# Optimization experiments

Hardware: AMD Instinct MI355X
Metric: run time of the kernel (lower is better)

Reference implementation:

```python
import jax, jax.numpy as jnp
import numpy as np

B, N, C, H, W = 32, 8, 256, 4, 4


def setup_inputs() -> dict:
    key = jax.random.key(0)
    k1, k2 = jax.random.split(key)
    pred = jax.random.normal(k1, (B, N, C, H, W), dtype=jnp.float32)
    gt = jax.random.normal(k2, (B, N, C, H, W), dtype=jnp.float32)
    return {"pred": pred, "gt": gt}


def reference(pred, gt):
    b, n, c, h, w = pred.shape
    M = b * n * h * w
    # (B,N,C,H,W) -> (B,N,H,W,C) -> (M, C)
    p = jnp.transpose(pred, (0, 1, 3, 4, 2)).reshape(M, c)
    # (B,N,C,H,W) -> (C,B,N,H,W) -> (C, M)
    g = jnp.transpose(gt, (2, 0, 1, 3, 4)).reshape(c, M)
    lossmat = p @ g  # (M, M) similarity matrix
    # CrossEntropy with target = arange(M): -mean(log_softmax diag)
    logp = jax.nn.log_softmax(lossmat, axis=1)
    loss = -jnp.mean(jnp.diagonal(logp))
    # accuracy (no grad in original)
    top1 = jnp.argmax(lossmat, axis=1)
    acc = jnp.mean((top1 == jnp.arange(M)).astype(jnp.float32)) * 100.0
    return (loss, acc)
```

## Files before the change

### kernel.cpp

```cpp
#include <hip/hip_runtime.h>
#include <cstdint>

typedef __bf16 bf16x8 __attribute__((ext_vector_type(8)));
typedef float floatx4 __attribute__((ext_vector_type(4)));


#define OFF_X     (0u)
#define OFF_Y     (2u*1024*1024)
#define OFF_PMAX  (4u*1024*1024)
#define OFF_PSUM  (5u*1024*1024)
#define OFF_DIAG  (6u*1024*1024)
#define OFF_LPART (OFF_DIAG + 16384u)
#define OFF_CPART (OFF_LPART + 256u)

#define AS1C(p) ((const __attribute__((address_space(1))) void*)(const void*)(p))
#define AS3(p)  ((__attribute__((address_space(3))) void*)(void*)(p))

__global__ __launch_bounds__(256) void transpose_stage(
    const float* __restrict__ pred, const float* __restrict__ gt,
    unsigned short* __restrict__ Xs, unsigned short* __restrict__ Ys) {
  int blk = blockIdx.x;
  const float* src;
  unsigned short* dst;
  int slab;
  if (blk < 256) { src = pred; dst = Xs; slab = blk; }
  else           { src = gt;   dst = Ys; slab = blk - 256; }
  const float* sb = src + slab * 4096;
  const int rb = slab >> 3, rowhi = slab & 7;
  const int t = threadIdx.x;
  #pragma unroll
  for (int half = 0; half < 2; ++half) {
    int c_ = half * 256 + t;
    int rowlo = c_ & 15;
    int quad  = (c_ >> 4) & 3;
    int kk    = (c_ >> 6) & 1;
    int s     = c_ >> 7;
    int k0 = s * 64 + kk * 32 + quad * 8;
    unsigned int packed[4];
    #pragma unroll
    for (int jj = 0; jj < 4; ++jj) {
      unsigned int lohi[2];
      #pragma unroll
      for (int e = 0; e < 2; ++e) {
        float f = sb[(k0 + jj * 2 + e) * 16 + rowlo];
        unsigned int u = __float_as_uint(f);
        lohi[e] = (u + 0x7FFFu + ((u >> 16) & 1u)) >> 16;
      }
      packed[jj] = lohi[0] | (lohi[1] << 16);
    }
    unsigned short* o = dst + rb * 32768 +
        (unsigned)(s * 1024 + kk * 512 + rowhi * 64 + quad * 16 + rowlo) * 8;
    uint4 v; v.x = packed[0]; v.y = packed[1]; v.z = packed[2]; v.w = packed[3];
    *reinterpret_cast<uint4*>(o) = v;
  }
}

__global__ __launch_bounds__(256) void gemm_softmax_partial(
    const unsigned short* __restrict__ Xs, const unsigned short* __restrict__ Ys,
    float* __restrict__ pmax, float* __restrict__ psum, float* __restrict__ diag) {
  __shared__ __align__(16) unsigned short As[8192];
  __shared__ __align__(16) unsigned short Bs[8192];
  const int t = threadIdx.x;
  const int wave = t >> 6, lane = t & 63;
  const int rg = wave >> 1, cg = wave & 1;
  const int bR = blockIdx.x, bC = blockIdx.y;
  const unsigned short* Ag = Xs + bR * 32768;
  const unsigned short* Bg = Ys + bC * 32768;

  floatx4 acc[4][4];
  const floatx4 zero = {0.f, 0.f, 0.f, 0.f};
  #pragma unroll
  for (int i = 0; i < 4; ++i)
    #pragma unroll
    for (int j = 0; j < 4; ++j) acc[i][j] = zero;

  for (int s = 0; s < 4; ++s) {
    #pragma unroll
    for (int it = 0; it < 4; ++it) {
      int chunk = it * 256 + t;
      __builtin_amdgcn_global_load_lds(AS1C(Ag + s * 8192 + chunk * 8),
                                       AS3(As + chunk * 8), 16, 0, 0);
      __builtin_amdgcn_global_load_lds(AS1C(Bg + s * 8192 + chunk * 8),
                                       AS3(Bs + chunk * 8), 16, 0, 0);
    }
    __syncthreads();
    #pragma unroll
    for (int kk = 0; kk < 2; ++kk) {
      bf16x8 a[4], b[4];
      #pragma unroll
      for (int fr = 0; fr < 4; ++fr)
        a[fr] = *reinterpret_cast<const bf16x8*>(
            As + (unsigned)(kk * 512 + (rg * 4 + fr) * 64 + lane) * 8);
      #pragma unroll
      for (int fc = 0; fc < 4; ++fc)
        b[fc] = *reinterpret_cast<const bf16x8*>(
            Bs + (unsigned)(kk * 512 + (cg * 4 + fc) * 64 + lane) * 8);
      #pragma unroll
      for (int fr = 0; fr < 4; ++fr)
        #pragma unroll
        for (int fc = 0; fc < 4; ++fc)
          acc[fr][fc] = __builtin_amdgcn_mfma_f32_16x16x32_bf16(
              a[fr], b[fc], acc[fr][fc], 0, 0, 0);
    }
    if (s < 3) __syncthreads();
  }

  const int quad = lane >> 4, lc = lane & 15;

  if (bR == bC && rg == cg) {
    #pragma unroll
    for (int fr = 0; fr < 4; ++fr)
      #pragma unroll
      for (int r = 0; r < 4; ++r)
        if (lc == quad * 4 + r)
          diag[bR * 128 + rg * 64 + fr * 16 + lc] = acc[fr][fr][r];
  }

  #pragma unroll
  for (int fr = 0; fr < 4; ++fr) {
    #pragma unroll
    for (int r = 0; r < 4; ++r) {
      float v0 = acc[fr][0][r], v1 = acc[fr][1][r];
      float v2 = acc[fr][2][r], v3 = acc[fr][3][r];
      float m = fmaxf(fmaxf(v0, v1), fmaxf(v2, v3));
      #pragma unroll
      for (int sh = 1; sh < 16; sh <<= 1) m = fmaxf(m, __shfl_xor(m, sh, 64));
      float ss = __expf(v0 - m) + __expf(v1 - m) +
                 __expf(v2 - m) + __expf(v3 - m);
      #pragma unroll
      for (int sh = 1; sh < 16; sh <<= 1) ss += __shfl_xor(ss, sh, 64);
      if (lc == 0) {
        int grow = bR * 128 + rg * 64 + fr * 16 + quad * 4 + r;
        int p = grow * 64 + bC * 2 + cg;
        pmax[p] = m; psum[p] = ss;
      }
    }
  }
}

__global__ __launch_bounds__(256) void combine_rows(
    const float* __restrict__ pmax, const float* __restrict__ psum,
    const float* __restrict__ diag,
    float* __restrict__ lpart, float* __restrict__ cpart) {
  int row = blockIdx.x * 256 + threadIdx.x;
  const float* pm = pmax + row * 64;
  const float* ps = psum + row * 64;
  float M = -3.4e38f;
  #pragma unroll 8
  for (int b = 0; b < 64; ++b) M = fmaxf(M, pm[b]);
  float S = 0.f;
  #pragma unroll 8
  for (int b = 0; b < 64; ++b) S += ps[b] * __expf(pm[b] - M);
  float d = diag[row];
  float lossr = logf(S) + M - d;
  float corr = (d == M) ? 1.f : 0.f;
  #pragma unroll
  for (int sh = 1; sh < 64; sh <<= 1) {
    lossr += __shfl_xor(lossr, sh, 64);
    corr  += __shfl_xor(corr,  sh, 64);
  }
  __shared__ float ls[4], cs[4];
  int wave = threadIdx.x >> 6, lane = threadIdx.x & 63;
  if (lane == 0) { ls[wave] = lossr; cs[wave] = corr; }
  __syncthreads();
  if (threadIdx.x == 0) {
    lpart[blockIdx.x] = ls[0] + ls[1] + ls[2] + ls[3];
    cpart[blockIdx.x] = cs[0] + cs[1] + cs[2] + cs[3];
  }
}

__global__ void finalize(const float* __restrict__ lpart,
                         const float* __restrict__ cpart,
                         float* __restrict__ out) {
  int t = threadIdx.x;
  float l = (t < 16) ? lpart[t] : 0.f;
  float c = (t < 16) ? cpart[t] : 0.f;
  #pragma unroll
  for (int sh = 1; sh < 16; sh <<= 1) {
    l += __shfl_xor(l, sh, 64);
    c += __shfl_xor(c, sh, 64);
  }
  if (t == 0) {
    out[0] = l * (1.f / 4096.f);
    out[1] = c * (100.f / 4096.f);
  }
}

extern "C" void kernel_launch(void* const* d_in, const int* in_sizes, int n_in,
                              void* d_out, int out_size, void* d_ws, size_t ws_size,
                              hipStream_t stream) {
  const float* pred = (const float*)d_in[0];
  const float* gt   = (const float*)d_in[1];
  char* w = (char*)d_ws;
  unsigned short* Xbf = (unsigned short*)(w + OFF_X);
  unsigned short* Ybf = (unsigned short*)(w + OFF_Y);
  float* pmax  = (float*)(w + OFF_PMAX);
  float* psum  = (float*)(w + OFF_PSUM);
  float* diag  = (float*)(w + OFF_DIAG);
  float* lpart = (float*)(w + OFF_LPART);
  float* cpart = (float*)(w + OFF_CPART);
  float* out   = (float*)d_out;

  transpose_stage<<<512, 256, 0, stream>>>(pred, gt, Xbf, Ybf);
  dim3 g1(32, 32);
  gemm_softmax_partial<<<g1, 256, 0, stream>>>(Xbf, Ybf, pmax, psum, diag);
  combine_rows<<<16, 256, 0, stream>>>(pmax, psum, diag, lpart, cpart);
  finalize<<<1, 64, 0, stream>>>(lpart, cpart, out);
}
```

Measured before the change: 94.22 us.

## Fuse row combine and finalize into GEMM kernel via last-block atomic counters

Removes the separate combine_rows and finalize launches. Each GEMM block bumps a per-row-block atomic counter, and the last block to finish a row block does the log-sum-exp combine for its 128 rows. A second counter then lets the final block sum the partials and write the outputs. The transpose kernel zeroes the counters, and the GEMM gains a launch_bounds occupancy hint. This saves two kernel launches in exchange for fences, atomics and a serial tail on the last blocks.

Result: slower. 123.6 us (+31.2%).

```diff
diff --git a/kernel.cpp b/kernel.cpp
--- a/kernel.cpp
+++ b/kernel.cpp
@@ -12,14 +12,18 @@
 #define OFF_DIAG  (6u*1024*1024)
 #define OFF_LPART (OFF_DIAG + 16384u)
 #define OFF_CPART (OFF_LPART + 256u)
+#define OFF_CNT   (OFF_CPART + 256u)
 
 #define AS1C(p) ((const __attribute__((address_space(1))) void*)(const void*)(p))
 #define AS3(p)  ((__attribute__((address_space(3))) void*)(void*)(p))
 
 __global__ __launch_bounds__(256) void transpose_stage(
     const float* __restrict__ pred, const float* __restrict__ gt,
-    unsigned short* __restrict__ Xs, unsigned short* __restrict__ Ys) {
+    unsigned short* __restrict__ Xs, unsigned short* __restrict__ Ys,
+    int* __restrict__ cnt) {
   int blk = blockIdx.x;
+  const int t = threadIdx.x;
+  if (blk == 0 && t < 33) cnt[t] = 0;
   const float* src;
   unsigned short* dst;
   int slab;
@@ -27,7 +31,6 @@
   else           { src = gt;   dst = Ys; slab = blk - 256; }
   const float* sb = src + slab * 4096;
   const int rb = slab >> 3, rowhi = slab & 7;
-  const int t = threadIdx.x;
   #pragma unroll
   for (int half = 0; half < 2; ++half) {
     int c_ = half * 256 + t;
@@ -55,11 +58,15 @@
   }
 }
 
-__global__ __launch_bounds__(256) void gemm_softmax_partial(
+__global__ __launch_bounds__(256, 4) void gemm_softmax_combine(
     const unsigned short* __restrict__ Xs, const unsigned short* __restrict__ Ys,
-    float* __restrict__ pmax, float* __restrict__ psum, float* __restrict__ diag) {
+    float* __restrict__ pmax, float* __restrict__ psum, float* __restrict__ diag,
+    float* __restrict__ lpart, float* __restrict__ cpart,
+    int* __restrict__ cnt, float* __restrict__ out) {
   __shared__ __align__(16) unsigned short As[8192];
   __shared__ __align__(16) unsigned short Bs[8192];
+  __shared__ float ls[4], cs[4];
+  __shared__ int lastflag;
   const int t = threadIdx.x;
   const int wave = t >> 6, lane = t & 63;
   const int rg = wave >> 1, cg = wave & 1;
@@ -136,53 +143,52 @@
       }
     }
   }
-}
-
-__global__ __launch_bounds__(256) void combine_rows(
-    const float* __restrict__ pmax, const float* __restrict__ psum,
-    const float* __restrict__ diag,
-    float* __restrict__ lpart, float* __restrict__ cpart) {
-  int row = blockIdx.x * 256 + threadIdx.x;
-  const float* pm = pmax + row * 64;
-  const float* ps = psum + row * 64;
-  float M = -3.4e38f;
-  #pragma unroll 8
-  for (int b = 0; b < 64; ++b) M = fmaxf(M, pm[b]);
-  float S = 0.f;
-  #pragma unroll 8
-  for (int b = 0; b < 64; ++b) S += ps[b] * __expf(pm[b] - M);
-  float d = diag[row];
-  float lossr = logf(S) + M - d;
-  float corr = (d == M) ? 1.f : 0.f;
+
+  __syncthreads();
+  if (t == 0) {
+    __threadfence();
+    int old = atomicAdd(cnt + bR, 1);
+    lastflag = (old == 31) ? 1 : 0;
+  }
+  __syncthreads();
+  if (!lastflag) return;
+
+  __threadfence();
+
+  float lossr = 0.f, corr = 0.f;
+  if (t < 128) {
+    int row = bR * 128 + t;
+    const float* pm = pmax + row * 64;
+    const float* ps = psum + row * 64;
+    float M = -3.4e38f;
+    #pragma unroll 8
+    for (int b = 0; b < 64; ++b) M = fmaxf(M, pm[b]);
+    float S = 0.f;
+    #pragma unroll 8
+    for (int b = 0; b < 64; ++b) S += ps[b] * __expf(pm[b] - M);
+    float d = diag[row];
+    lossr = logf(S) + M - d;
+    corr = (d == M) ? 1.f : 0.f;
+  }
   #pragma unroll
   for (int sh = 1; sh < 64; sh <<= 1) {
     lossr += __shfl_xor(lossr, sh, 64);
     corr  += __shfl_xor(corr,  sh, 64);
   }
-  __shared__ float ls[4], cs[4];
-  int wave = threadIdx.x >> 6, lane = threadIdx.x & 63;
   if (lane == 0) { ls[wave] = lossr; cs[wave] = corr; }
   __syncthreads();
-  if (threadIdx.x == 0) {
-    lpart[blockIdx.x] = ls[0] + ls[1] + ls[2] + ls[3];
-    cpart[blockIdx.x] = cs[0] + cs[1] + cs[2] + cs[3];
-  }
-}
-
-__global__ void finalize(const float* __restrict__ lpart,
-                         const float* __restrict__ cpart,
-                         float* __restrict__ out) {
-  int t = threadIdx.x;
-  float l = (t < 16) ? lpart[t] : 0.f;
-  float c = (t < 16) ? cpart[t] : 0.f;
-  #pragma unroll
-  for (int sh = 1; sh < 16; sh <<= 1) {
-    l += __shfl_xor(l, sh, 64);
-    c += __shfl_xor(c, sh, 64);
-  }
   if (t == 0) {
-    out[0] = l * (1.f / 4096.f);
-    out[1] = c * (100.f / 4096.f);
+    lpart[bR] = ls[0] + ls[1] + ls[2] + ls[3];
+    cpart[bR] = cs[0] + cs[1] + cs[2] + cs[3];
+    __threadfence();
+    int old2 = atomicAdd(cnt + 32, 1);
+    if (old2 == 31) {
+      __threadfence();
+      float L = 0.f, C = 0.f;
+      for (int i = 0; i < 32; ++i) { L += lpart[i]; C += cpart[i]; }
+      out[0] = L * (1.f / 4096.f);
+      out[1] = C * (100.f / 4096.f);
+    }
   }
 }
 
@@ -199,11 +205,11 @@
   float* diag  = (float*)(w + OFF_DIAG);
   float* lpart = (float*)(w + OFF_LPART);
   float* cpart = (float*)(w + OFF_CPART);
+  int*   cnt   = (int*)(w + OFF_CNT);
   float* out   = (float*)d_out;
 
-  transpose_stage<<<512, 256, 0, stream>>>(pred, gt, Xbf, Ybf);
+  transpose_stage<<<512, 256, 0, stream>>>(pred, gt, Xbf, Ybf, cnt);
   dim3 g1(32, 32);
-  gemm_softmax_partial<<<g1, 256, 0, stream>>>(Xbf, Ybf, pmax, psum, diag);
-  combine_rows<<<16, 256, 0, stream>>>(pmax, psum, diag, lpart, cpart);
-  finalize<<<1, 64, 0, stream>>>(lpart, cpart, out);
+  gemm_softmax_combine<<<g1, 256, 0, stream>>>(Xbf, Ybf, pmax, psum, diag,
+                                               lpart, cpart, cnt, out);
 }
```

## Enlarge GEMM tiles to 256x256 with double-buffered LDS and fuse finalize

Applied to the files above, without the earlier changes.

The GEMM moves from 128x128 tiles with 4 waves to 256x256 tiles with 8 waves per block, so each block reuses more operand data, and it double-buffers the LDS loads so the next K-slab is fetched while the current one runs on MFMA. The separate finalize kernel is removed: the last combine_rows block, detected through an atomic counter reset in the transpose kernel, sums the partials and writes the output. The grid drops to 256 blocks, which may underfill the CUs, and LDS use rises to 128KB per block.

New measurement: 94.06 us. About the same (-0.2%).

```diff
diff --git a/kernel.cpp b/kernel.cpp
--- a/kernel.cpp
+++ b/kernel.cpp
@@ -12,14 +12,18 @@
 #define OFF_DIAG  (6u*1024*1024)
 #define OFF_LPART (OFF_DIAG + 16384u)
 #define OFF_CPART (OFF_LPART + 256u)
+#define OFF_CNT   (OFF_CPART + 256u)
 
 #define AS1C(p) ((const __attribute__((address_space(1))) void*)(const void*)(p))
 #define AS3(p)  ((__attribute__((address_space(3))) void*)(void*)(p))
 
 __global__ __launch_bounds__(256) void transpose_stage(
     const float* __restrict__ pred, const float* __restrict__ gt,
-    unsigned short* __restrict__ Xs, unsigned short* __restrict__ Ys) {
+    unsigned short* __restrict__ Xs, unsigned short* __restrict__ Ys,
+    int* __restrict__ cnt) {
   int blk = blockIdx.x;
+  const int t = threadIdx.x;
+  if (blk == 0 && t < 33) cnt[t] = 0;
   const float* src;
   unsigned short* dst;
   int slab;
@@ -27,7 +31,6 @@
   else           { src = gt;   dst = Ys; slab = blk - 256; }
   const float* sb = src + slab * 4096;
   const int rb = slab >> 3, rowhi = slab & 7;
-  const int t = threadIdx.x;
   #pragma unroll
   for (int half = 0; half < 2; ++half) {
     int c_ = half * 256 + t;
@@ -55,69 +58,83 @@
   }
 }
 
-__global__ __launch_bounds__(256) void gemm_softmax_partial(
+__global__ __launch_bounds__(512) void gemm_softmax_partial(
     const unsigned short* __restrict__ Xs, const unsigned short* __restrict__ Ys,
     float* __restrict__ pmax, float* __restrict__ psum, float* __restrict__ diag) {
-  __shared__ __align__(16) unsigned short As[8192];
-  __shared__ __align__(16) unsigned short Bs[8192];
+  __shared__ __align__(16) unsigned short As[2][16384];
+  __shared__ __align__(16) unsigned short Bs[2][16384];
   const int t = threadIdx.x;
   const int wave = t >> 6, lane = t & 63;
-  const int rg = wave >> 1, cg = wave & 1;
-  const int bR = blockIdx.x, bC = blockIdx.y;
-  const unsigned short* Ag = Xs + bR * 32768;
-  const unsigned short* Bg = Ys + bC * 32768;
-
-  floatx4 acc[4][4];
+  const int rg = wave >> 2, cg = wave & 3;
+  const int bC = blockIdx.x, bR = blockIdx.y;
+  const unsigned short* Ag = Xs + bR * 65536;
+  const unsigned short* Bg = Ys + bC * 65536;
+
+  floatx4 acc[8][4];
   const floatx4 zero = {0.f, 0.f, 0.f, 0.f};
   #pragma unroll
-  for (int i = 0; i < 4; ++i)
+  for (int i = 0; i < 8; ++i)
     #pragma unroll
     for (int j = 0; j < 4; ++j) acc[i][j] = zero;
 
+  auto STAGE = [&](int buf, int s) {
+    #pragma unroll
+    for (int it = 0; it < 4; ++it) {
+      int chunk = it * 512 + t;
+      int half = chunk >> 10, w_ = chunk & 1023;
+      __builtin_amdgcn_global_load_lds(
+          AS1C(Ag + half * 32768 + s * 8192 + w_ * 8),
+          AS3(&As[buf][(unsigned)chunk * 8]), 16, 0, 0);
+      __builtin_amdgcn_global_load_lds(
+          AS1C(Bg + half * 32768 + s * 8192 + w_ * 8),
+          AS3(&Bs[buf][(unsigned)chunk * 8]), 16, 0, 0);
+    }
+  };
+
+  STAGE(0, 0);
+  __syncthreads();
+  int buf = 0;
   for (int s = 0; s < 4; ++s) {
-    #pragma unroll
-    for (int it = 0; it < 4; ++it) {
-      int chunk = it * 256 + t;
-      __builtin_amdgcn_global_load_lds(AS1C(Ag + s * 8192 + chunk * 8),
-                                       AS3(As + chunk * 8), 16, 0, 0);
-      __builtin_amdgcn_global_load_lds(AS1C(Bg + s * 8192 + chunk * 8),
-                                       AS3(Bs + chunk * 8), 16, 0, 0);
-    }
-    __syncthreads();
+    if (s < 3) STAGE(buf ^ 1, s + 1);
     #pragma unroll
     for (int kk = 0; kk < 2; ++kk) {
-      bf16x8 a[4], b[4];
-      #pragma unroll
-      for (int fr = 0; fr < 4; ++fr)
-        a[fr] = *reinterpret_cast<const bf16x8*>(
-            As + (unsigned)(kk * 512 + (rg * 4 + fr) * 64 + lane) * 8);
-      #pragma unroll
-      for (int fc = 0; fc < 4; ++fc)
+      bf16x8 b[4];
+      #pragma unroll
+      for (int fc = 0; fc < 4; ++fc) {
+        int gc = cg * 4 + fc;
         b[fc] = *reinterpret_cast<const bf16x8*>(
-            Bs + (unsigned)(kk * 512 + (cg * 4 + fc) * 64 + lane) * 8);
-      #pragma unroll
-      for (int fr = 0; fr < 4; ++fr)
+            &Bs[buf][(unsigned)((gc >> 3) * 8192 + kk * 4096 +
+                                (gc & 7) * 512 + lane * 8)]);
+      }
+      #pragma unroll
+      for (int fr = 0; fr < 8; ++fr) {
+        bf16x8 a = *reinterpret_cast<const bf16x8*>(
+            &As[buf][(unsigned)(rg * 8192 + kk * 4096 + fr * 512 + lane * 8)]);
         #pragma unroll
         for (int fc = 0; fc < 4; ++fc)
           acc[fr][fc] = __builtin_amdgcn_mfma_f32_16x16x32_bf16(
-              a[fr], b[fc], acc[fr][fc], 0, 0, 0);
-    }
-    if (s < 3) __syncthreads();
+              a, b[fc], acc[fr][fc], 0, 0, 0);
+      }
+    }
+    if (s < 3) { __syncthreads(); buf ^= 1; }
   }
 
   const int quad = lane >> 4, lc = lane & 15;
 
-  if (bR == bC && rg == cg) {
-    #pragma unroll
-    for (int fr = 0; fr < 4; ++fr)
-      #pragma unroll
-      for (int r = 0; r < 4; ++r)
-        if (lc == quad * 4 + r)
-          diag[bR * 128 + rg * 64 + fr * 16 + lc] = acc[fr][fr][r];
-  }
-
-  #pragma unroll
-  for (int fr = 0; fr < 4; ++fr) {
+  if (bR == bC) {
+    #pragma unroll
+    for (int fr = 0; fr < 8; ++fr) {
+      if (cg == 2 * rg + (fr >> 2)) {
+        #pragma unroll
+        for (int r = 0; r < 4; ++r)
+          if (lc == quad * 4 + r)
+            diag[bR * 256 + rg * 128 + fr * 16 + lc] = acc[fr][fr & 3][r];
+      }
+    }
+  }
+
+  #pragma unroll
+  for (int fr = 0; fr < 8; ++fr) {
     #pragma unroll
     for (int r = 0; r < 4; ++r) {
       float v0 = acc[fr][0][r], v1 = acc[fr][1][r];
@@ -130,8 +147,8 @@
       #pragma unroll
       for (int sh = 1; sh < 16; sh <<= 1) ss += __shfl_xor(ss, sh, 64);
       if (lc == 0) {
-        int grow = bR * 128 + rg * 64 + fr * 16 + quad * 4 + r;
-        int p = grow * 64 + bC * 2 + cg;
+        int grow = bR * 256 + rg * 128 + fr * 16 + quad * 4 + r;
+        int p = grow * 64 + bC * 4 + cg;
         pmax[p] = m; psum[p] = ss;
       }
     }
@@ -141,7 +158,8 @@
 __global__ __launch_bounds__(256) void combine_rows(
     const float* __restrict__ pmax, const float* __restrict__ psum,
     const float* __restrict__ diag,
-    float* __restrict__ lpart, float* __restrict__ cpart) {
+    float* __restrict__ lpart, float* __restrict__ cpart,
+    int* __restrict__ cnt, float* __restrict__ out) {
   int row = blockIdx.x * 256 + threadIdx.x;
   const float* pm = pmax + row * 64;
   const float* ps = psum + row * 64;
@@ -166,23 +184,14 @@
   if (threadIdx.x == 0) {
     lpart[blockIdx.x] = ls[0] + ls[1] + ls[2] + ls[3];
     cpart[blockIdx.x] = cs[0] + cs[1] + cs[2] + cs[3];
-  }
-}
-
-__global__ void finalize(const float* __restrict__ lpart,
-                         const float* __restrict__ cpart,
-                         float* __restrict__ out) {
-  int t = threadIdx.x;
-  float l = (t < 16) ? lpart[t] : 0.f;
-  float c = (t < 16) ? cpart[t] : 0.f;
-  #pragma unroll
-  for (int sh = 1; sh < 16; sh <<= 1) {
-    l += __shfl_xor(l, sh, 64);
-    c += __shfl_xor(c, sh, 64);
-  }
-  if (t == 0) {
-    out[0] = l * (1.f / 4096.f);
-    out[1] = c * (100.f / 4096.f);
+    __threadfence();
+    if (atomicAdd(cnt, 1) == 15) {
+      __threadfence();
+      float L = 0.f, C = 0.f;
+      for (int i = 0; i < 16; ++i) { L += lpart[i]; C += cpart[i]; }
+      out[0] = L * (1.f / 4096.f);
+      out[1] = C * (100.f / 4096.f);
+    }
   }
 }
 
@@ -199,11 +208,11 @@
   float* diag  = (float*)(w + OFF_DIAG);
   float* lpart = (float*)(w + OFF_LPART);
   float* cpart = (float*)(w + OFF_CPART);
+  int*   cnt   = (int*)(w + OFF_CNT);
   float* out   = (float*)d_out;
 
-  transpose_stage<<<512, 256, 0, stream>>>(pred, gt, Xbf, Ybf);
-  dim3 g1(32, 32);
-  gemm_softmax_partial<<<g1, 256, 0, stream>>>(Xbf, Ybf, pmax, psum, diag);
-  combine_rows<<<16, 256, 0, stream>>>(pmax, psum, diag, lpart, cpart);
-  finalize<<<1, 64, 0, stream>>>(lpart, cpart, out);
-}
+  transpose_stage<<<512, 256, 0, stream>>>(pred, gt, Xbf, Ybf, cnt);
+  dim3 g1(16, 16);
+  gemm_softmax_partial<<<g1, 512, 0, stream>>>(Xbf, Ybf, pmax, psum, diag);
+  combine_rows<<<16, 256, 0, stream>>>(pmax, psum, diag, lpart, cpart, cnt, out);
+}
```
